# Performance work log

Measured on AMD Instinct MI355X. Metric: run time of the kernel, lower is better.

## Reference

```python
import jax, jax.numpy as jnp
import numpy as np

N_ITER = 3
N_GRID = 2048
N_SENSORS = 64
N_SNAP = 128
BATCH = 128
HID = 32
VAR_NOISE = 0.1


def setup_inputs() -> dict:
    key = jax.random.key(0)
    ks = jax.random.split(key, 8)
    data = jax.random.normal(ks[0], (BATCH, N_SENSORS, N_SNAP), dtype=jnp.float32)
    A = jax.random.normal(ks[1], (N_SENSORS, N_GRID), dtype=jnp.float32)
    # per-(iteration, gridpoint) MLP: 3 -> HID -> HID -> 1 (ReLU, bias, no BN, no skip)
    s1 = 1.0 / np.sqrt(3.0)
    s2 = 1.0 / np.sqrt(HID)
    W1 = jax.random.normal(ks[2], (N_ITER, N_GRID, 3, HID), dtype=jnp.float32) * s1
    b1 = jnp.zeros((N_ITER, N_GRID, HID), dtype=jnp.float32)
    W2 = jax.random.normal(ks[3], (N_ITER, N_GRID, HID, HID), dtype=jnp.float32) * s2
    b2 = jnp.zeros((N_ITER, N_GRID, HID), dtype=jnp.float32)
    W3 = jax.random.normal(ks[4], (N_ITER, N_GRID, HID), dtype=jnp.float32) * s2
    b3 = jnp.zeros((N_ITER, N_GRID), dtype=jnp.float32)
    return {"data": data, "A": A, "W1": W1, "b1": b1, "W2": W2, "b2": b2, "W3": W3, "b3": b3}


def _iteration(g, data, A, W1, b1, W2, b2, W3, b3):
    B, m, _ = data.shape
    eye = VAR_NOISE * jnp.eye(m, dtype=data.dtype)
    # cov_yy[b] = A diag(gamma_b) A^T + var_noise I   -> [B, m, m]
    cov = jnp.einsum('bg,mg,ng->bmn', g, A, A) + eye
    t1 = jnp.linalg.solve(cov, data)                          # [B, m, T]
    t2 = jnp.linalg.solve(cov, jnp.broadcast_to(A, (B,) + A.shape))  # [B, m, G]
    T2 = jnp.abs(jnp.einsum('mg,bmg->bg', A, t2))             # diag(A^T Sigma^{-1} A)
    T1 = jnp.mean(jnp.einsum('mg,bmt->bgt', A, t1) ** 2, axis=-1)    # [B, G]
    x = jnp.stack([T1, T2, g], axis=-1)                       # [B, G, 3]
    h = jax.nn.relu(jnp.einsum('bgf,gfh->bgh', x, W1) + b1)
    h = jax.nn.relu(jnp.einsum('bgh,ghk->bgk', h, W2) + b2)
    return jnp.einsum('bgh,gh->bg', h, W3) + b3               # new gamma [B, G]


def reference(data, A, W1, b1, W2, b2, W3, b3):
    B = data.shape[0]
    g = jnp.ones((B, N_GRID), dtype=jnp.float32)
    for i in range(N_ITER):
        g = _iteration(g, data, A, W1[i], b1[i], W2[i], b2[i], W3[i], b3[i])
    return g
```

## Files before the change

### kernel.cpp

```cpp
#include <hip/hip_runtime.h>

#define NB 128
#define NM 64
#define NT 128
#define NG 2048
#define NH 32


__global__ __launch_bounds__(256) void k_init(float* __restrict__ g) {
    g[blockIdx.x * 256 + threadIdx.x] = 1.0f;
}

__global__ __launch_bounds__(256) void k_D(const float* __restrict__ data,
                                           float* __restrict__ D) {
    __shared__ float sd[64 * 133];
    int b = blockIdx.x, t = threadIdx.x;
    const float* db = data + (size_t)b * 8192;
    for (int idx = t; idx < 8192; idx += 256)
        sd[(idx >> 7) * 133 + (idx & 127)] = db[idx];
    __syncthreads();
    int i0 = (t & 15) * 4, j0 = (t >> 4) * 4;
    float acc[4][4];
#pragma unroll
    for (int r = 0; r < 4; ++r)
#pragma unroll
        for (int c = 0; c < 4; ++c) acc[r][c] = 0.f;
    for (int tt = 0; tt < 128; ++tt) {
        float av[4], bv[4];
#pragma unroll
        for (int r = 0; r < 4; ++r) av[r] = sd[(i0 + r) * 133 + tt];
#pragma unroll
        for (int c = 0; c < 4; ++c) bv[c] = sd[(j0 + c) * 133 + tt];
#pragma unroll
        for (int r = 0; r < 4; ++r)
#pragma unroll
            for (int c = 0; c < 4; ++c) acc[r][c] += av[r] * bv[c];
    }
    float* Db = D + (size_t)b * 4096;
#pragma unroll
    for (int r = 0; r < 4; ++r)
#pragma unroll
        for (int c = 0; c < 4; ++c)
            Db[(i0 + r) * 64 + j0 + c] = acc[r][c] * (1.0f / 128.0f);
}

__global__ __launch_bounds__(256) void k_cov(const float* __restrict__ A,
                                             const float* __restrict__ g,
                                             float* __restrict__ p0,
                                             float* __restrict__ p1,
                                             float* __restrict__ p2,
                                             float* __restrict__ p3) {
    int b = blockIdx.x >> 2, q = blockIdx.x & 3, t = threadIdx.x;
    int goff = q * 512;
    __shared__ float sA[32 * 64];
    __shared__ float sAg[32 * 64];
    __shared__ float sg[512];
    for (int idx = t; idx < 512; idx += 256)
        sg[idx] = g[(size_t)b * NG + goff + idx];
    float acc[4][4];
#pragma unroll
    for (int r = 0; r < 4; ++r)
#pragma unroll
        for (int c = 0; c < 4; ++c) acc[r][c] = 0.f;
    int i0 = (t & 15) * 4, j0 = (t >> 4) * 4;
    int m = t >> 2, gs = (t & 3) * 8;
    __syncthreads();
    for (int ch = 0; ch < 16; ++ch) {
        const float* Ar = A + (size_t)m * NG + goff + ch * 32 + gs;
        float4 v0 = *(const float4*)Ar;
        float4 v1 = *(const float4*)(Ar + 4);
        __syncthreads();
        sA[(gs + 0) * 64 + m] = v0.x; sAg[(gs + 0) * 64 + m] = v0.x * sg[ch * 32 + gs + 0];
        sA[(gs + 1) * 64 + m] = v0.y; sAg[(gs + 1) * 64 + m] = v0.y * sg[ch * 32 + gs + 1];
        sA[(gs + 2) * 64 + m] = v0.z; sAg[(gs + 2) * 64 + m] = v0.z * sg[ch * 32 + gs + 2];
        sA[(gs + 3) * 64 + m] = v0.w; sAg[(gs + 3) * 64 + m] = v0.w * sg[ch * 32 + gs + 3];
        sA[(gs + 4) * 64 + m] = v1.x; sAg[(gs + 4) * 64 + m] = v1.x * sg[ch * 32 + gs + 4];
        sA[(gs + 5) * 64 + m] = v1.y; sAg[(gs + 5) * 64 + m] = v1.y * sg[ch * 32 + gs + 5];
        sA[(gs + 6) * 64 + m] = v1.z; sAg[(gs + 6) * 64 + m] = v1.z * sg[ch * 32 + gs + 6];
        sA[(gs + 7) * 64 + m] = v1.w; sAg[(gs + 7) * 64 + m] = v1.w * sg[ch * 32 + gs + 7];
        __syncthreads();
#pragma unroll
        for (int gg = 0; gg < 32; ++gg) {
            float4 av = *(const float4*)&sAg[gg * 64 + i0];
            float4 bv = *(const float4*)&sA[gg * 64 + j0];
            acc[0][0] += av.x * bv.x; acc[0][1] += av.x * bv.y;
            acc[0][2] += av.x * bv.z; acc[0][3] += av.x * bv.w;
            acc[1][0] += av.y * bv.x; acc[1][1] += av.y * bv.y;
            acc[1][2] += av.y * bv.z; acc[1][3] += av.y * bv.w;
            acc[2][0] += av.z * bv.x; acc[2][1] += av.z * bv.y;
            acc[2][2] += av.z * bv.z; acc[2][3] += av.z * bv.w;
            acc[3][0] += av.w * bv.x; acc[3][1] += av.w * bv.y;
            acc[3][2] += av.w * bv.z; acc[3][3] += av.w * bv.w;
        }
    }
    float* dst = (q == 0 ? p0 : q == 1 ? p1 : q == 2 ? p2 : p3) + (size_t)b * 4096;
#pragma unroll
    for (int r = 0; r < 4; ++r)
#pragma unroll
        for (int c = 0; c < 4; ++c)
            dst[(i0 + r) * 64 + j0 + c] = acc[r][c];
}

#define GJSTEP(RB, WB, KK)                                                    \
    {                                                                         \
        const float* krow = (RB) + (KK) * 68;                                 \
        const float* rowp = (RB) + lane * 68;                                 \
        float4 prow[16], own[16];                                             \
        _Pragma("unroll")                                                     \
        for (int bj = 0; bj < 16; ++bj) prow[bj] = *(const float4*)(krow + 4 * bj); \
        _Pragma("unroll")                                                     \
        for (int bj = 0; bj < 16; ++bj) own[bj] = *(const float4*)(rowp + 4 * bj);  \
        float p = krow[KK];                                                   \
        float c = rowp[KK];                                                   \
        float ps = (__builtin_fabsf(p) < 1e-12f) ? (p >= 0.f ? 1e-12f : -1e-12f) : p; \
        float pinv = __builtin_amdgcn_rcpf(ps);                               \
        bool isk = (lane == (KK));                                            \
        float n  = isk ? 0.0f : 1.0f;                                         \
        float m2 = isk ? -pinv : c * pinv;                                    \
        float* wr = (WB) + lane * 68;                                         \
        _Pragma("unroll")                                                     \
        for (int bj = 0; bj < 16; ++bj) {                                     \
            float4 res;                                                       \
            res.x = own[bj].x * n - m2 * prow[bj].x;                          \
            res.y = own[bj].y * n - m2 * prow[bj].y;                          \
            res.z = own[bj].z * n - m2 * prow[bj].z;                          \
            res.w = own[bj].w * n - m2 * prow[bj].w;                          \
            *(float4*)(wr + 4 * bj) = res;                                    \
        }                                                                     \
        wr[KK] = isk ? pinv : -m2;   \
    }

#define GEMMT(Ash, Bsh)                                                       \
    {                                                                         \
        _Pragma("unroll")                                                     \
        for (int rr = 0; rr < 4; ++rr)                                        \
            for (int cc = 0; cc < 4; ++cc) acc[rr][cc] = 0.f;                 \
        _Pragma("unroll 4")                                                   \
        for (int kk = 0; kk < 64; kk += 4) {                                  \
            float4 av[4], bv[4];                                              \
            _Pragma("unroll")                                                 \
            for (int qq = 0; qq < 4; ++qq) {                                  \
                av[qq] = *(const float4*)((Ash) + (kk + qq) * 68 + i0);       \
                bv[qq] = *(const float4*)((Bsh) + (kk + qq) * 68 + j0);       \
            }                                                                 \
            _Pragma("unroll")                                                 \
            for (int qq = 0; qq < 4; ++qq) {                                  \
                acc[0][0] += av[qq].x * bv[qq].x; acc[0][1] += av[qq].x * bv[qq].y; \
                acc[0][2] += av[qq].x * bv[qq].z; acc[0][3] += av[qq].x * bv[qq].w; \
                acc[1][0] += av[qq].y * bv[qq].x; acc[1][1] += av[qq].y * bv[qq].y; \
                acc[1][2] += av[qq].y * bv[qq].z; acc[1][3] += av[qq].y * bv[qq].w; \
                acc[2][0] += av[qq].z * bv[qq].x; acc[2][1] += av[qq].z * bv[qq].y; \
                acc[2][2] += av[qq].z * bv[qq].z; acc[2][3] += av[qq].z * bv[qq].w; \
                acc[3][0] += av[qq].w * bv[qq].x; acc[3][1] += av[qq].w * bv[qq].y; \
                acc[3][2] += av[qq].w * bv[qq].z; acc[3][3] += av[qq].w * bv[qq].w; \
            }                                                                 \
        }                                                                     \
    }

__global__ __launch_bounds__(256, 1) void k_invpost(const float* p0, const float* p1,
                                                    const float* p2, const float* p3,
                                                    const float* Dws,
                                                    float* Sbuf, float* Mbuf) {
    __shared__ float sX[64 * 68];
    __shared__ float sA[64 * 68];
    __shared__ float sR[64 * 68];
    int t = threadIdx.x, b = blockIdx.x;
    size_t boff = (size_t)b * 4096;

    float4 dreg[4];
#pragma unroll
    for (int u = 0; u < 4; ++u)
        dreg[u] = ((const float4*)(Dws + boff))[u * 256 + t];

#pragma unroll
    for (int u = 0; u < 4; ++u) {
        int idx = u * 1024 + t * 4;
        int i = idx >> 6, j = idx & 63;
        float4 v0 = *(const float4*)(p0 + boff + idx);
        float4 v1 = *(const float4*)(p1 + boff + idx);
        float4 v2 = *(const float4*)(p2 + boff + idx);
        float4 v3 = *(const float4*)(p3 + boff + idx);
        float4 v = make_float4((v0.x + v1.x) + (v2.x + v3.x),
                               (v0.y + v1.y) + (v2.y + v3.y),
                               (v0.z + v1.z) + (v2.z + v3.z),
                               (v0.w + v1.w) + (v2.w + v3.w));
        int d = i - j;
        if (d >= 0 && d < 4) (&v.x)[d] += 0.1f;
        *(float4*)(sX + i * 68 + j) = v;
        *(float4*)(sA + i * 68 + j) = v;
    }
    __syncthreads();

    if (t < 64) {
        int lane = t;
#pragma unroll 1
        for (int k2 = 0; k2 < 32; ++k2) {
            GJSTEP(sX, sR, 2 * k2);
            GJSTEP(sR, sX, 2 * k2 + 1);
        }
    }
    __syncthreads();

    int i0 = (t & 15) * 4, j0 = (t >> 4) * 4;
    float acc[4][4];

    GEMMT(sA, sX);
#pragma unroll
    for (int rr = 0; rr < 4; ++rr)
#pragma unroll
        for (int cc = 0; cc < 4; ++cc)
            sR[(i0 + rr) * 68 + j0 + cc] =
                ((i0 + rr) == (j0 + cc) ? 2.0f : 0.0f) - acc[rr][cc];
    __syncthreads();

    GEMMT(sX, sR);
#pragma unroll
    for (int rr = 0; rr < 4; ++rr) {
#pragma unroll
        for (int cc = 0; cc < 4; ++cc)
            sA[(i0 + rr) * 68 + j0 + cc] = acc[rr][cc];
        *(float4*)(Sbuf + boff + (i0 + rr) * 64 + j0) =
            make_float4(acc[rr][0], acc[rr][1], acc[rr][2], acc[rr][3]);
    }
    __syncthreads();

#pragma unroll
    for (int u = 0; u < 4; ++u) {
        int idx = u * 1024 + t * 4;
        *(float4*)(sX + (idx >> 6) * 68 + (idx & 63)) = dreg[u];
    }
    __syncthreads();

    GEMMT(sX, sA);
    __syncthreads();
#pragma unroll
    for (int rr = 0; rr < 4; ++rr)
#pragma unroll
        for (int cc = 0; cc < 4; ++cc)
            sR[(i0 + rr) * 68 + j0 + cc] = acc[rr][cc];
    __syncthreads();

    GEMMT(sA, sR);
#pragma unroll
    for (int rr = 0; rr < 4; ++rr)
        *(float4*)(Mbuf + boff + (i0 + rr) * 64 + j0) =
            make_float4(acc[rr][0], acc[rr][1], acc[rr][2], acc[rr][3]);
}

__global__ __launch_bounds__(256, 1) void k_feat(const float* __restrict__ A,
                                                 const float* __restrict__ Sbuf,
                                                 const float* __restrict__ Mbuf,
                                                 float* __restrict__ T1,
                                                 float* __restrict__ T2) {
    __shared__ float sS[4096];
    __shared__ float sM[4096];
    __shared__ float sa[8192];
    int t = threadIdx.x;
    int b = blockIdx.x >> 3, tile = blockIdx.x & 7;
    const float* Abase = A + tile * 256;
    {
        const float4* S4 = (const float4*)(Sbuf + (size_t)b * 4096);
        const float4* M4 = (const float4*)(Mbuf + (size_t)b * 4096);
#pragma unroll
        for (int u = 0; u < 4; ++u) {
            ((float4*)sS)[u * 256 + t] = S4[u * 256 + t];
            ((float4*)sM)[u * 256 + t] = M4[u * 256 + t];
        }
#pragma unroll
        for (int u = 0; u < 8; ++u) {
            int idx = u * 1024 + t * 4;
            int kk = idx >> 8, gl = idx & 255;
            *(float4*)(sa + idx) = *(const float4*)(Abase + (size_t)kk * NG + gl);
        }
    }
    int iq = t >> 4, gq = t & 15;
    int i0 = iq * 4;
    float accS[4][16], accM[4][16];
#pragma unroll
    for (int r = 0; r < 4; ++r)
#pragma unroll
        for (int c = 0; c < 16; ++c) { accS[r][c] = 0.f; accM[r][c] = 0.f; }
    __syncthreads();

#pragma unroll 1
    for (int p = 0; p < 2; ++p) {
        if (p) {
            __syncthreads();
#pragma unroll
            for (int u = 0; u < 8; ++u) {
                int idx = u * 1024 + t * 4;
                int kk = idx >> 8, gl = idx & 255;
                *(float4*)(sa + idx) =
                    *(const float4*)(Abase + (size_t)(32 + kk) * NG + gl);
            }
            __syncthreads();
        }
#pragma unroll 2
        for (int kk = 0; kk < 32; ++kk) {
            int k = p * 32 + kk;
            float4 sf = *(const float4*)(sS + k * 64 + i0);
            float4 mf = *(const float4*)(sM + k * 64 + i0);
            const float* ak = sa + kk * 256 + gq * 4;
            float4 a0 = *(const float4*)(ak);
            float4 a1 = *(const float4*)(ak + 64);
            float4 a2 = *(const float4*)(ak + 128);
            float4 a3 = *(const float4*)(ak + 192);
            float af[16] = {a0.x, a0.y, a0.z, a0.w, a1.x, a1.y, a1.z, a1.w,
                            a2.x, a2.y, a2.z, a2.w, a3.x, a3.y, a3.z, a3.w};
#pragma unroll
            for (int r = 0; r < 4; ++r) {
                float sr = (&sf.x)[r];
                float mr = (&mf.x)[r];
#pragma unroll
                for (int c = 0; c < 16; ++c) {
                    accS[r][c] += sr * af[c];
                    accM[r][c] += mr * af[c];
                }
            }
        }
    }

    float pS[16], pM[16];
#pragma unroll
    for (int c = 0; c < 16; ++c) { pS[c] = 0.f; pM[c] = 0.f; }
#pragma unroll
    for (int r = 0; r < 4; ++r) {
        const float* arp = A + (size_t)(i0 + r) * NG + tile * 256 + gq * 4;
        float4 b0 = *(const float4*)(arp);
        float4 b1 = *(const float4*)(arp + 64);
        float4 b2 = *(const float4*)(arp + 128);
        float4 b3 = *(const float4*)(arp + 192);
        float ar[16] = {b0.x, b0.y, b0.z, b0.w, b1.x, b1.y, b1.z, b1.w,
                        b2.x, b2.y, b2.z, b2.w, b3.x, b3.y, b3.z, b3.w};
#pragma unroll
        for (int c = 0; c < 16; ++c) {
            pS[c] += ar[c] * accS[r][c];
            pM[c] += ar[c] * accM[r][c];
        }
    }
    __syncthreads();

#pragma unroll
    for (int ch = 0; ch < 4; ++ch) {
        *(float4*)(sS + iq * 256 + ch * 64 + gq * 4) =
            make_float4(pS[ch * 4], pS[ch * 4 + 1], pS[ch * 4 + 2], pS[ch * 4 + 3]);
        *(float4*)(sM + iq * 256 + ch * 64 + gq * 4) =
            make_float4(pM[ch * 4], pM[ch * 4 + 1], pM[ch * 4 + 2], pM[ch * 4 + 3]);
    }
    __syncthreads();

    float sumS = 0.f, sumM = 0.f;
#pragma unroll
    for (int q = 0; q < 16; ++q) {
        sumS += sS[q * 256 + t];
        sumM += sM[q * 256 + t];
    }
    size_t base = (size_t)b * NG + tile * 256 + t;
    T2[base] = fabsf(sumS);
    T1[base] = sumM;
}

__global__ __launch_bounds__(256) void k_mlp(const float* __restrict__ T1,
                                             const float* __restrict__ T2,
                                             const float* __restrict__ gcur,
                                             const float* __restrict__ W1,
                                             const float* __restrict__ b1,
                                             const float* __restrict__ W2,
                                             const float* __restrict__ b2,
                                             const float* __restrict__ W3,
                                             const float* __restrict__ b3,
                                             int it, float* __restrict__ out) {
    __shared__ float w[8 * 1220];
    int t = threadIdx.x, g0 = blockIdx.x * 8;
    for (int gl = 0; gl < 8; ++gl) {
        size_t gi = (size_t)it * NG + g0 + gl;
        float* wd = &w[gl * 1220];
        if (t < 96) wd[t] = W1[gi * 96 + t];
        else if (t < 128) wd[t] = b1[gi * 32 + (t - 96)];
        const float* w2 = W2 + gi * 1024;
#pragma unroll
        for (int u = 0; u < 4; ++u) wd[128 + u * 256 + t] = w2[u * 256 + t];
        if (t < 32) wd[1152 + t] = b2[gi * 32 + t];
        else if (t < 64) wd[1184 + (t - 32)] = W3[gi * 32 + (t - 32)];
        else if (t == 64) wd[1216] = b3[gi];
    }
    __syncthreads();
    int gl = t & 7, gg = g0 + gl;
    const float* wd = &w[gl * 1220];
    for (int bp = 0; bp < 4; ++bp) {
        int bb = (t >> 3) + bp * 32;
        size_t xo = (size_t)bb * NG + gg;
        float x0 = T1[xo], x1 = T2[xo], x2 = gcur[xo];
        float h1[32];
#pragma unroll
        for (int k = 0; k < 32; k += 4) {
            float4 wa = *(const float4*)(wd + k);
            float4 wb = *(const float4*)(wd + 32 + k);
            float4 wc = *(const float4*)(wd + 64 + k);
            float4 bv = *(const float4*)(wd + 96 + k);
            h1[k + 0] = fmaxf(0.f, x0 * wa.x + x1 * wb.x + x2 * wc.x + bv.x);
            h1[k + 1] = fmaxf(0.f, x0 * wa.y + x1 * wb.y + x2 * wc.y + bv.y);
            h1[k + 2] = fmaxf(0.f, x0 * wa.z + x1 * wb.z + x2 * wc.z + bv.z);
            h1[k + 3] = fmaxf(0.f, x0 * wa.w + x1 * wb.w + x2 * wc.w + bv.w);
        }
        float acc = wd[1216];
#pragma unroll
        for (int k = 0; k < 32; k += 4) {
            float4 hb = *(const float4*)(wd + 1152 + k);
            float v0 = hb.x, v1 = hb.y, v2 = hb.z, v3 = hb.w;
#pragma unroll
            for (int j = 0; j < 32; ++j) {
                float4 w2v = *(const float4*)(wd + 128 + j * 32 + k);
                v0 += h1[j] * w2v.x; v1 += h1[j] * w2v.y;
                v2 += h1[j] * w2v.z; v3 += h1[j] * w2v.w;
            }
            float4 w3v = *(const float4*)(wd + 1184 + k);
            acc += fmaxf(0.f, v0) * w3v.x + fmaxf(0.f, v1) * w3v.y +
                   fmaxf(0.f, v2) * w3v.z + fmaxf(0.f, v3) * w3v.w;
        }
        out[xo] = acc;
    }
}

extern "C" void kernel_launch(void* const* d_in, const int* in_sizes, int n_in,
                              void* d_out, int out_size, void* d_ws, size_t ws_size,
                              hipStream_t stream) {
    const float* data = (const float*)d_in[0];
    const float* A    = (const float*)d_in[1];
    const float* W1   = (const float*)d_in[2];
    const float* b1   = (const float*)d_in[3];
    const float* W2   = (const float*)d_in[4];
    const float* b2   = (const float*)d_in[5];
    const float* W3   = (const float*)d_in[6];
    const float* b3   = (const float*)d_in[7];
    float* out = (float*)d_out;
    float* ws = (float*)d_ws;

    float* D  = ws;
    float* P0 = ws + 524288;
    float* P1 = ws + 1048576;
    float* P2 = ws + 1572864;
    float* P3 = ws + 2097152;
    float* T1 = ws + 2621440;
    float* T2 = ws + 2883584;
    float* gA = ws + 3145728;
    float* gB = ws + 3407872;

    k_init<<<dim3(1024), dim3(256), 0, stream>>>(gA);
    k_D<<<dim3(128), dim3(256), 0, stream>>>(data, D);

    float* gc = gA;
    float* gn = gB;
    for (int it = 0; it < 3; ++it) {
        k_cov<<<dim3(512), dim3(256), 0, stream>>>(A, gc, P0, P1, P2, P3);
        k_invpost<<<dim3(128), dim3(256), 0, stream>>>(P0, P1, P2, P3, D, P0, P1);
        k_feat<<<dim3(1024), dim3(256), 0, stream>>>(A, P0, P1, T1, T2);
        float* dst = (it == 2) ? out : gn;
        k_mlp<<<dim3(256), dim3(256), 0, stream>>>(T1, T2, gc, W1, b1, W2, b2, W3, b3, it, dst);
        float* tmp = gc; gc = gn; gn = tmp;
    }
}
```

Before: 615.3 us.

## Double-buffer A tiles in k_feat and batch four samples per thread in k_mlp

k_feat now streams A through two small shared buffers in 8-row chunks, with a register prefetch of the next chunk issued before the current chunk's FMAs, replacing one large synchronous reload. This lowers LDS use and hides global-load latency, at the cost of one barrier per chunk. k_mlp processes all four batch samples per thread together so each W2 float4 read from LDS is reused four times, which raises register pressure; launch bounds are set to one block per SM.

```diff
diff --git a/kernel.cpp b/kernel.cpp
--- a/kernel.cpp
+++ b/kernel.cpp
@@ -254,7 +254,7 @@
                                                  float* __restrict__ T2) {
     __shared__ float sS[4096];
     __shared__ float sM[4096];
-    __shared__ float sa[8192];
+    __shared__ float sa[2][2048];
     int t = threadIdx.x;
     int b = blockIdx.x >> 3, tile = blockIdx.x & 7;
     const float* Abase = A + tile * 256;
@@ -267,10 +267,10 @@
             ((float4*)sM)[u * 256 + t] = M4[u * 256 + t];
         }
 #pragma unroll
-        for (int u = 0; u < 8; ++u) {
+        for (int u = 0; u < 2; ++u) {
             int idx = u * 1024 + t * 4;
             int kk = idx >> 8, gl = idx & 255;
-            *(float4*)(sa + idx) = *(const float4*)(Abase + (size_t)kk * NG + gl);
+            *(float4*)(&sa[0][0] + idx) = *(const float4*)(Abase + (size_t)kk * NG + gl);
         }
     }
     int iq = t >> 4, gq = t & 15;
@@ -283,24 +283,23 @@
     __syncthreads();
 
 #pragma unroll 1
-    for (int p = 0; p < 2; ++p) {
-        if (p) {
-            __syncthreads();
-#pragma unroll
-            for (int u = 0; u < 8; ++u) {
-                int idx = u * 1024 + t * 4;
-                int kk = idx >> 8, gl = idx & 255;
-                *(float4*)(sa + idx) =
-                    *(const float4*)(Abase + (size_t)(32 + kk) * NG + gl);
-            }
-            __syncthreads();
-        }
-#pragma unroll 2
-        for (int kk = 0; kk < 32; ++kk) {
-            int k = p * 32 + kk;
+    for (int p = 0; p < 8; ++p) {
+        const float* buf = &sa[p & 1][0];
+        float4 st0, st1;
+        int i0s = 0, i1s = 0;
+        if (p < 7) {
+            int kb = (p + 1) * 8;
+            i0s = t * 4;
+            i1s = 1024 + t * 4;
+            st0 = *(const float4*)(Abase + (size_t)(kb + (i0s >> 8)) * NG + (i0s & 255));
+            st1 = *(const float4*)(Abase + (size_t)(kb + (i1s >> 8)) * NG + (i1s & 255));
+        }
+#pragma unroll
+        for (int kk = 0; kk < 8; ++kk) {
+            int k = p * 8 + kk;
             float4 sf = *(const float4*)(sS + k * 64 + i0);
             float4 mf = *(const float4*)(sM + k * 64 + i0);
-            const float* ak = sa + kk * 256 + gq * 4;
+            const float* ak = buf + kk * 256 + gq * 4;
             float4 a0 = *(const float4*)(ak);
             float4 a1 = *(const float4*)(ak + 64);
             float4 a2 = *(const float4*)(ak + 128);
@@ -318,6 +317,12 @@
                 }
             }
         }
+        if (p < 7) {
+            float* nb = &sa[(p + 1) & 1][0];
+            *(float4*)(nb + i0s) = st0;
+            *(float4*)(nb + i1s) = st1;
+        }
+        __syncthreads();
     }
 
     float pS[16], pM[16];
@@ -360,16 +365,16 @@
     T1[base] = sumM;
 }
 
-__global__ __launch_bounds__(256) void k_mlp(const float* __restrict__ T1,
-                                             const float* __restrict__ T2,
-                                             const float* __restrict__ gcur,
-                                             const float* __restrict__ W1,
-                                             const float* __restrict__ b1,
-                                             const float* __restrict__ W2,
-                                             const float* __restrict__ b2,
-                                             const float* __restrict__ W3,
-                                             const float* __restrict__ b3,
-                                             int it, float* __restrict__ out) {
+__global__ __launch_bounds__(256, 1) void k_mlp(const float* __restrict__ T1,
+                                                const float* __restrict__ T2,
+                                                const float* __restrict__ gcur,
+                                                const float* __restrict__ W1,
+                                                const float* __restrict__ b1,
+                                                const float* __restrict__ W2,
+                                                const float* __restrict__ b2,
+                                                const float* __restrict__ W3,
+                                                const float* __restrict__ b3,
+                                                int it, float* __restrict__ out) {
     __shared__ float w[8 * 1220];
     int t = threadIdx.x, g0 = blockIdx.x * 8;
     for (int gl = 0; gl < 8; ++gl) {
@@ -387,39 +392,64 @@
     __syncthreads();
     int gl = t & 7, gg = g0 + gl;
     const float* wd = &w[gl * 1220];
-    for (int bp = 0; bp < 4; ++bp) {
-        int bb = (t >> 3) + bp * 32;
-        size_t xo = (size_t)bb * NG + gg;
-        float x0 = T1[xo], x1 = T2[xo], x2 = gcur[xo];
-        float h1[32];
-#pragma unroll
-        for (int k = 0; k < 32; k += 4) {
-            float4 wa = *(const float4*)(wd + k);
-            float4 wb = *(const float4*)(wd + 32 + k);
-            float4 wc = *(const float4*)(wd + 64 + k);
-            float4 bv = *(const float4*)(wd + 96 + k);
-            h1[k + 0] = fmaxf(0.f, x0 * wa.x + x1 * wb.x + x2 * wc.x + bv.x);
-            h1[k + 1] = fmaxf(0.f, x0 * wa.y + x1 * wb.y + x2 * wc.y + bv.y);
-            h1[k + 2] = fmaxf(0.f, x0 * wa.z + x1 * wb.z + x2 * wc.z + bv.z);
-            h1[k + 3] = fmaxf(0.f, x0 * wa.w + x1 * wb.w + x2 * wc.w + bv.w);
-        }
-        float acc = wd[1216];
-#pragma unroll
-        for (int k = 0; k < 32; k += 4) {
-            float4 hb = *(const float4*)(wd + 1152 + k);
-            float v0 = hb.x, v1 = hb.y, v2 = hb.z, v3 = hb.w;
-#pragma unroll
-            for (int j = 0; j < 32; ++j) {
-                float4 w2v = *(const float4*)(wd + 128 + j * 32 + k);
-                v0 += h1[j] * w2v.x; v1 += h1[j] * w2v.y;
-                v2 += h1[j] * w2v.z; v3 += h1[j] * w2v.w;
+    int b0 = t >> 3;
+
+    float x0[4], x1[4], x2[4];
+#pragma unroll
+    for (int c = 0; c < 4; ++c) {
+        size_t xo = (size_t)(b0 + c * 32) * NG + gg;
+        x0[c] = T1[xo]; x1[c] = T2[xo]; x2[c] = gcur[xo];
+    }
+
+    float h1[4][32];
+#pragma unroll
+    for (int k = 0; k < 32; k += 4) {
+        float4 wa = *(const float4*)(wd + k);
+        float4 wb = *(const float4*)(wd + 32 + k);
+        float4 wc = *(const float4*)(wd + 64 + k);
+        float4 bv = *(const float4*)(wd + 96 + k);
+#pragma unroll
+        for (int c = 0; c < 4; ++c) {
+            h1[c][k + 0] = fmaxf(0.f, x0[c] * wa.x + x1[c] * wb.x + x2[c] * wc.x + bv.x);
+            h1[c][k + 1] = fmaxf(0.f, x0[c] * wa.y + x1[c] * wb.y + x2[c] * wc.y + bv.y);
+            h1[c][k + 2] = fmaxf(0.f, x0[c] * wa.z + x1[c] * wb.z + x2[c] * wc.z + bv.z);
+            h1[c][k + 3] = fmaxf(0.f, x0[c] * wa.w + x1[c] * wb.w + x2[c] * wc.w + bv.w);
+        }
+    }
+
+    float acc[4];
+    float b3v = wd[1216];
+#pragma unroll
+    for (int c = 0; c < 4; ++c) acc[c] = b3v;
+#pragma unroll 1
+    for (int k = 0; k < 32; k += 4) {
+        float4 hb = *(const float4*)(wd + 1152 + k);
+        float v[4][4];
+#pragma unroll
+        for (int c = 0; c < 4; ++c) {
+            v[c][0] = hb.x; v[c][1] = hb.y; v[c][2] = hb.z; v[c][3] = hb.w;
+        }
+#pragma unroll
+        for (int j = 0; j < 32; ++j) {
+            float4 w2v = *(const float4*)(wd + 128 + j * 32 + k);
+#pragma unroll
+            for (int c = 0; c < 4; ++c) {
+                v[c][0] += h1[c][j] * w2v.x;
+                v[c][1] += h1[c][j] * w2v.y;
+                v[c][2] += h1[c][j] * w2v.z;
+                v[c][3] += h1[c][j] * w2v.w;
             }
-            float4 w3v = *(const float4*)(wd + 1184 + k);
-            acc += fmaxf(0.f, v0) * w3v.x + fmaxf(0.f, v1) * w3v.y +
-                   fmaxf(0.f, v2) * w3v.z + fmaxf(0.f, v3) * w3v.w;
-        }
-        out[xo] = acc;
-    }
+        }
+        float4 w3v = *(const float4*)(wd + 1184 + k);
+#pragma unroll
+        for (int c = 0; c < 4; ++c) {
+            acc[c] += fmaxf(0.f, v[c][0]) * w3v.x + fmaxf(0.f, v[c][1]) * w3v.y +
+                      fmaxf(0.f, v[c][2]) * w3v.z + fmaxf(0.f, v[c][3]) * w3v.w;
+        }
+    }
+#pragma unroll
+    for (int c = 0; c < 4; ++c)
+        out[(size_t)(b0 + c * 32) * NG + gg] = acc[c];
 }
 
 extern "C" void kernel_launch(void* const* d_in, const int* in_sizes, int n_in,
```

Result: no change. 627.2 us (+1.9%).
